# Optimization experiments

Hardware: AMD Instinct MI355X
Metric: run time of the kernel (lower is better)

Reference implementation:

```python
import jax, jax.numpy as jnp
import numpy as np
import math

D_MODEL = 2048
N_HEADS = 16
HEAD_DIM = D_MODEL // N_HEADS
ROPE_THETA = 10000.0
EPS = 1e-5


def _rope_cos_sin(seq_len, dim, theta):
    inv_freq = 1.0 / theta ** (jnp.arange(0, dim, 2, dtype=jnp.float32) / dim)  # [dim/2]
    t = jnp.arange(seq_len, dtype=jnp.float32)
    freqs = jnp.outer(t, inv_freq)  # [S, dim/2]
    return jnp.cos(freqs), jnp.sin(freqs)


def _apply_rope(x, cos, sin):
    # x: [B, S, H, D]; pairs (even, odd) rotated by angle freqs[s, d/2]
    xs = x.reshape(x.shape[:-1] + (x.shape[-1] // 2, 2))
    x0, x1 = xs[..., 0], xs[..., 1]
    c = cos[None, :, None, :]
    s = sin[None, :, None, :]
    out = jnp.stack([x0 * c - x1 * s, x0 * s + x1 * c], axis=-1)
    return out.reshape(x.shape)


def _layernorm(x, w, eps):
    # LayerNorm over last dim, no bias
    mu = jnp.mean(x, axis=-1, keepdims=True)
    var = jnp.mean(jnp.square(x - mu), axis=-1, keepdims=True)
    return (x - mu) * jax.lax.rsqrt(var + eps) * w


def setup_inputs() -> dict:
    key = jax.random.key(0)
    ks = jax.random.split(key, 5)
    B, S = 2, 2048
    w_std = math.sqrt(1.0 / D_MODEL)  # ~xavier for square matrices
    return {
        "x": jax.random.normal(ks[0], (B, S, D_MODEL), dtype=jnp.float32),
        "wq": jax.random.normal(ks[1], (D_MODEL, D_MODEL), dtype=jnp.float32) * w_std,
        "wk": jax.random.normal(ks[2], (D_MODEL, D_MODEL), dtype=jnp.float32) * w_std,
        "wv": jax.random.normal(ks[3], (D_MODEL, D_MODEL), dtype=jnp.float32) * w_std,
        "wo": jax.random.normal(ks[4], (D_MODEL, D_MODEL), dtype=jnp.float32) * w_std,
        "q_norm_w": jnp.ones((HEAD_DIM,), dtype=jnp.float32),
        "k_norm_w": jnp.ones((HEAD_DIM,), dtype=jnp.float32),
        "window_size": 1024,
    }


def reference(x, wq, wk, wv, wo, q_norm_w, k_norm_w, window_size):
    B, S, _ = x.shape
    # bias-free projections (torch Linear: x @ W.T)
    q = (x @ wq.T).reshape(B, S, N_HEADS, HEAD_DIM)
    k = (x @ wk.T).reshape(B, S, N_HEADS, HEAD_DIM)
    v = (x @ wv.T).reshape(B, S, N_HEADS, HEAD_DIM)

    cos, sin = _rope_cos_sin(S, HEAD_DIM, ROPE_THETA)
    q = _apply_rope(q, cos, sin)
    k = _apply_rope(k, cos, sin)

    # per-head QK LayerNorm (no bias)
    q = _layernorm(q, q_norm_w, EPS)
    k = _layernorm(k, k_norm_w, EPS)

    scale = 1.0 / math.sqrt(HEAD_DIM)
    scores = jnp.einsum("bqhd,bkhd->bhqk", q, k) * scale  # [B,H,S,S]

    # sliding-window causal mask: attend to j in [i - window, i]
    i = jnp.arange(S)[:, None]
    j = jnp.arange(S)[None, :]
    allowed = (j <= i) & (j >= i - window_size)
    scores = jnp.where(allowed, scores, -jnp.inf)

    attn = jax.nn.softmax(scores, axis=-1)
    out = jnp.einsum("bhqk,bkhd->bqhd", attn, v).reshape(B, S, D_MODEL)
    return out @ wo.T
```

## Files before the change

kernel.cpp:

```cpp
#include <hip/hip_runtime.h>

typedef __bf16 bfv8 __attribute__((ext_vector_type(8)));
typedef float f32x4 __attribute__((ext_vector_type(4)));

#define DMODEL 2048
#define NHEADS 16
#define HEADD 128
#define SEQ 2048
#define BATCH 2
#define MROWS (BATCH * SEQ)

__device__ __forceinline__ unsigned short f2bf(float f) {
    unsigned int x = __float_as_uint(f);
    x += 0x7fffu + ((x >> 16) & 1u);
    return (unsigned short)(x >> 16);
}
__device__ __forceinline__ float bf2f(unsigned short u) {
    return __uint_as_float((unsigned int)u << 16);
}
__device__ __forceinline__ unsigned int pk2(float a, float b) {
    return (unsigned int)f2bf(a) | ((unsigned int)f2bf(b) << 16);
}

__global__ __launch_bounds__(256) void cvt_all(const float* __restrict__ x,
                                               const float* __restrict__ wq,
                                               const float* __restrict__ wk,
                                               const float* __restrict__ wv,
                                               const float* __restrict__ wo,
                                               unsigned short* __restrict__ dst) {
    int bid = blockIdx.x;
    const float* s;
    int off;
    if (bid < 8192)       { s = x;  off = bid; }
    else if (bid < 12288) { s = wq; off = bid - 8192; }
    else if (bid < 16384) { s = wk; off = bid - 12288; }
    else if (bid < 20480) { s = wv; off = bid - 16384; }
    else                  { s = wo; off = bid - 20480; }
    int i = off * 1024 + threadIdx.x * 4;
    float4 v = *(const float4*)(s + i);
    ushort4 o;
    o.x = f2bf(v.x); o.y = f2bf(v.y); o.z = f2bf(v.z); o.w = f2bf(v.w);
    *(ushort4*)(dst + (size_t)bid * 1024 + threadIdx.x * 4) = o;
}

template <int CPRL, int ITERS>
__device__ __forceinline__ void stage_n(const unsigned short* __restrict__ gbase,
                                        unsigned short* lds, size_t strideShorts,
                                        int wave, int lane) {
#pragma unroll
    for (int i = 0; i < ITERS; ++i) {
        int L = wave * (64 * ITERS) + i * 64 + lane;
        int m = L >> CPRL, c = L & ((1 << CPRL) - 1);
        int g = c ^ (m & 7);
        const unsigned short* gp = gbase + (size_t)m * strideShorts + g * 8;
        __builtin_amdgcn_global_load_lds(
            (const __attribute__((address_space(1))) unsigned int*)gp,
            (__attribute__((address_space(3))) unsigned int*)(lds + (size_t)(wave * (64 * ITERS) + i * 64) * 8),
            16, 0, 0);
    }
}

#define GBK 64

__global__ __launch_bounds__(256) void gemm_qkv(const unsigned short* __restrict__ A,
                                                const unsigned short* __restrict__ Bw,
                                                unsigned short* __restrict__ Qb,
                                                unsigned short* __restrict__ Kb,
                                                unsigned short* __restrict__ VT) {
    __shared__ __align__(16) unsigned short As[128 * 64];
    __shared__ __align__(16) unsigned short Bs[128 * 64];
    const int K = DMODEL;
    int tid  = threadIdx.x;
    int bm   = blockIdx.y * 128, bn = blockIdx.x * 128;
    int wave = tid >> 6, lane = tid & 63;
    int wm   = (wave >> 1) * 64, wn = (wave & 1) * 64;
    int lr   = lane & 15, lg = lane >> 4;

    f32x4 acc[4][4];
    f32x4 z = {0.f, 0.f, 0.f, 0.f};
#pragma unroll
    for (int i = 0; i < 4; ++i)
#pragma unroll
        for (int j = 0; j < 4; ++j) acc[i][j] = z;

    const unsigned short* Ab = A  + (size_t)bm * K;
    const unsigned short* Bb = Bw + (size_t)bn * K;

    for (int k0 = 0; k0 < K; k0 += GBK) {
        __syncthreads();
        stage_n<3, 4>(Ab + k0, As, K, wave, lane);
        stage_n<3, 4>(Bb + k0, Bs, K, wave, lane);
        __syncthreads();
#pragma unroll
        for (int kk = 0; kk < GBK; kk += 32) {
            int ck = (kk >> 3) + lg;
            bfv8 af[4], bf[4];
#pragma unroll
            for (int i = 0; i < 4; ++i)
                af[i] = *(const bfv8*)&As[(wm + i * 16 + lr) * 64 + (ck ^ (lr & 7)) * 8];
#pragma unroll
            for (int j = 0; j < 4; ++j)
                bf[j] = *(const bfv8*)&Bs[(wn + j * 16 + lr) * 64 + (ck ^ (lr & 7)) * 8];
#pragma unroll
            for (int i = 0; i < 4; ++i)
#pragma unroll
                for (int j = 0; j < 4; ++j)
                    acc[i][j] = __builtin_amdgcn_mfma_f32_16x16x32_bf16(af[i], bf[j], acc[i][j], 0, 0, 0);
        }
    }
    int orow0 = bm + wm + lg * 4;
    int region = bn >> 11;
    int nloc   = bn & 2047;
    if (region < 2) {
        unsigned short* C = region ? Kb : Qb;
#pragma unroll
        for (int i = 0; i < 4; ++i)
#pragma unroll
            for (int j = 0; j < 4; ++j)
#pragma unroll
                for (int r = 0; r < 4; ++r)
                    C[(size_t)(orow0 + i * 16 + r) * DMODEL + nloc + wn + j * 16 + lr] = f2bf(acc[i][j][r]);
    } else {
#pragma unroll
        for (int i = 0; i < 4; ++i) {
            int row = orow0 + i * 16;
            int bb = row >> 11, ss = row & (SEQ - 1);
#pragma unroll
            for (int j = 0; j < 4; ++j) {
                int col = nloc + wn + j * 16 + lr;
                int hh = col >> 7, dd = col & (HEADD - 1);
                ushort4 o4;
                o4.x = f2bf(acc[i][j][0]);
                o4.y = f2bf(acc[i][j][1]);
                o4.z = f2bf(acc[i][j][2]);
                o4.w = f2bf(acc[i][j][3]);
                *(ushort4*)(VT + ((size_t)((bb * NHEADS + hh) * HEADD + dd)) * SEQ + ss) = o4;
            }
        }
    }
}

__global__ __launch_bounds__(256) void gemm_bt(const unsigned short* __restrict__ A,
                                               const unsigned short* __restrict__ Bw,
                                               float* __restrict__ C,
                                               int M, int N, int K) {
    __shared__ __align__(16) unsigned short As[128 * 64];
    __shared__ __align__(16) unsigned short Bs[128 * 64];
    int tid  = threadIdx.x;
    int bm   = blockIdx.y * 128, bn = blockIdx.x * 128;
    int wave = tid >> 6, lane = tid & 63;
    int wm   = (wave >> 1) * 64, wn = (wave & 1) * 64;
    int lr   = lane & 15, lg = lane >> 4;

    f32x4 acc[4][4];
    f32x4 z = {0.f, 0.f, 0.f, 0.f};
#pragma unroll
    for (int i = 0; i < 4; ++i)
#pragma unroll
        for (int j = 0; j < 4; ++j) acc[i][j] = z;

    const unsigned short* Ab = A  + (size_t)bm * K;
    const unsigned short* Bb = Bw + (size_t)bn * K;

    for (int k0 = 0; k0 < K; k0 += GBK) {
        __syncthreads();
        stage_n<3, 4>(Ab + k0, As, K, wave, lane);
        stage_n<3, 4>(Bb + k0, Bs, K, wave, lane);
        __syncthreads();
#pragma unroll
        for (int kk = 0; kk < GBK; kk += 32) {
            int ck = (kk >> 3) + lg;
            bfv8 af[4], bf[4];
#pragma unroll
            for (int i = 0; i < 4; ++i)
                af[i] = *(const bfv8*)&As[(wm + i * 16 + lr) * 64 + (ck ^ (lr & 7)) * 8];
#pragma unroll
            for (int j = 0; j < 4; ++j)
                bf[j] = *(const bfv8*)&Bs[(wn + j * 16 + lr) * 64 + (ck ^ (lr & 7)) * 8];
#pragma unroll
            for (int i = 0; i < 4; ++i)
#pragma unroll
                for (int j = 0; j < 4; ++j)
                    acc[i][j] = __builtin_amdgcn_mfma_f32_16x16x32_bf16(af[i], bf[j], acc[i][j], 0, 0, 0);
        }
    }
    int orow0 = bm + wm + lg * 4;
    int ocol0 = bn + wn + lr;
#pragma unroll
    for (int i = 0; i < 4; ++i)
#pragma unroll
        for (int j = 0; j < 4; ++j)
#pragma unroll
            for (int r = 0; r < 4; ++r)
                C[(size_t)(orow0 + i * 16 + r) * N + ocol0 + j * 16] = acc[i][j][r];
}

__global__ __launch_bounds__(256) void rope_ln_ip(unsigned short* __restrict__ qt,
                                                  unsigned short* __restrict__ kt,
                                                  const float* __restrict__ qw,
                                                  const float* __restrict__ kw) {
    int which = blockIdx.y;
    unsigned short* t = which ? kt : qt;
    const float* w = which ? kw : qw;
    float scale = which ? 1.0f : 0.08838834764831845f;
    int gr   = blockIdx.x * 4 + (threadIdx.x >> 6);
    int lane = threadIdx.x & 63;
    int m = gr >> 4;
    int h = gr & 15;
    int s = m & (SEQ - 1);
    unsigned short* p = t + (size_t)m * DMODEL + h * HEADD + lane * 2;
    ushort2 xv = *(const ushort2*)p;
    float x0 = bf2f(xv.x), x1 = bf2f(xv.y);
    float inv = powf(10000.0f, -(float)lane * (1.0f / 64.0f));
    float ang = (float)s * inv;
    float sn, c;
    sincosf(ang, &sn, &c);
    float y0 = x0 * c - x1 * sn;
    float y1 = x0 * sn + x1 * c;
    float sum = y0 + y1;
    float sq  = y0 * y0 + y1 * y1;
#pragma unroll
    for (int o = 32; o >= 1; o >>= 1) {
        sum += __shfl_xor(sum, o);
        sq  += __shfl_xor(sq, o);
    }
    float mu  = sum * (1.0f / 128.0f);
    float var = sq * (1.0f / 128.0f) - mu * mu;
    float rs  = rsqrtf(var + 1e-5f) * scale;
    float2 wv = *(const float2*)(w + lane * 2);
    ushort2 ov;
    ov.x = f2bf((y0 - mu) * rs * wv.x);
    ov.y = f2bf((y1 - mu) * rs * wv.y);
    *(ushort2*)p = ov;
}

#define AQT 64
#define AKT 64

__global__ __launch_bounds__(256) void attn_mfma(const unsigned short* __restrict__ qb,
                                                 const unsigned short* __restrict__ kb,
                                                 const unsigned short* __restrict__ vt,
                                                 unsigned short* __restrict__ ob,
                                                 const int* __restrict__ wptr) {
    __shared__ __align__(16) unsigned short Ks[64 * 128];
    __shared__ __align__(16) unsigned short Vs[128 * 64];
    __shared__ __align__(16) unsigned short Ps[4 * 16 * 64];
    int tid  = threadIdx.x;
    int wq   = tid >> 6, lane = tid & 63;
    int lm   = lane & 15, lg = lane >> 4;
    int lm7  = lm & 7;
    int gid  = blockIdx.x;
    int xcd  = gid & 7, slot = gid >> 3;
    int bh   = xcd * 4 + (slot >> 5);
    int b    = bh >> 4, h = bh & 15;
    int q0   = (31 - (slot & 31)) * AQT;
    int W    = *wptr;
    unsigned short* PsW = &Ps[wq * 1024];

    bfv8 qa[4];
    {
        const unsigned short* qp = qb + (size_t)(b * SEQ + q0 + wq * 16 + lm) * DMODEL + h * HEADD + lg * 8;
#pragma unroll
        for (int kk = 0; kk < 4; ++kk) qa[kk] = *(const bfv8*)(qp + kk * 32);
    }

    f32x4 o[8];
    f32x4 z = {0.f, 0.f, 0.f, 0.f};
#pragma unroll
    for (int n = 0; n < 8; ++n) o[n] = z;
    float mrow = -1e30f, lrow = 0.f;

    const unsigned short* kbase = kb + (size_t)(b * SEQ) * DMODEL + h * HEADD;
    const unsigned short* vbase = vt + (size_t)((b * NHEADS + h) * HEADD) * SEQ;

    int kt_lo = max(0, q0 - W) & ~(AKT - 1);
    int qi = q0 + wq * 16 + lm;

    for (int kt = kt_lo; kt < q0 + AQT; kt += AKT) {
        __syncthreads();
        stage_n<4, 4>(kbase + (size_t)kt * DMODEL, Ks, DMODEL, wq, lane);
        stage_n<3, 4>(vbase + kt, Vs, SEQ, wq, lane);
        __syncthreads();

        f32x4 s[4];
#pragma unroll
        for (int j = 0; j < 4; ++j) s[j] = z;
#pragma unroll
        for (int kk = 0; kk < 4; ++kk) {
#pragma unroll
            for (int j = 0; j < 4; ++j) {
                int ck = (kk * 4 + lg) ^ lm7;
                bfv8 af = *(const bfv8*)&Ks[(j * 16 + lm) * 128 + ck * 8];
                s[j] = __builtin_amdgcn_mfma_f32_16x16x32_bf16(af, qa[kk], s[j], 0, 0, 0);
            }
        }
        if ((kt + 63 >= q0) || (kt < q0 + 63 - W)) {
#pragma unroll
            for (int j = 0; j < 4; ++j) {
                int kj0 = kt + j * 16 + lg * 4;
#pragma unroll
                for (int r = 0; r < 4; ++r) {
                    bool ok = (kj0 + r <= qi) && (kj0 + r >= qi - W);
                    s[j][r] = ok ? s[j][r] : -1e30f;
                }
            }
        }
        float mx = -1e30f;
#pragma unroll
        for (int j = 0; j < 4; ++j)
#pragma unroll
            for (int r = 0; r < 4; ++r) mx = fmaxf(mx, s[j][r]);
        mx = fmaxf(mx, __shfl_xor(mx, 16));
        mx = fmaxf(mx, __shfl_xor(mx, 32));
        float mnew  = fmaxf(mrow, mx);
        float alpha = __expf(mrow - mnew);
        mrow = mnew;
        float ls = 0.f;
#pragma unroll
        for (int j = 0; j < 4; ++j) {
            float p0 = __expf(s[j][0] - mnew);
            float p1 = __expf(s[j][1] - mnew);
            float p2 = __expf(s[j][2] - mnew);
            float p3 = __expf(s[j][3] - mnew);
            ls += (p0 + p1) + (p2 + p3);
            int c0 = (j * 2 + (lg >> 1)) ^ lm7;
            uint2 wv;
            wv.x = pk2(p0, p1);
            wv.y = pk2(p2, p3);
            *(uint2*)&PsW[lm * 64 + c0 * 8 + (lg & 1) * 4] = wv;
        }
        ls += __shfl_xor(ls, 16);
        ls += __shfl_xor(ls, 32);
        lrow = lrow * alpha + ls;
        float al[4];
#pragma unroll
        for (int r = 0; r < 4; ++r) al[r] = __shfl(alpha, lg * 4 + r);
#pragma unroll
        for (int n = 0; n < 8; ++n)
#pragma unroll
            for (int r = 0; r < 4; ++r) o[n][r] *= al[r];
#pragma unroll
        for (int k2 = 0; k2 < 2; ++k2) {
            int cc = (k2 * 4 + lg) ^ lm7;
            bfv8 pa = *(const bfv8*)&PsW[lm * 64 + cc * 8];
#pragma unroll
            for (int n = 0; n < 8; ++n) {
                bfv8 vf = *(const bfv8*)&Vs[(n * 16 + lm) * 64 + cc * 8];
                o[n] = __builtin_amdgcn_mfma_f32_16x16x32_bf16(pa, vf, o[n], 0, 0, 0);
            }
        }
    }
    float linv[4];
#pragma unroll
    for (int r = 0; r < 4; ++r) linv[r] = 1.0f / __shfl(lrow, lg * 4 + r);
    int qrow = q0 + wq * 16 + lg * 4;
    unsigned short* op = ob + (size_t)(b * SEQ + qrow) * DMODEL + h * HEADD + lm;
#pragma unroll
    for (int n = 0; n < 8; ++n)
#pragma unroll
        for (int r = 0; r < 4; ++r)
            op[(size_t)r * DMODEL + n * 16] = f2bf(o[n][r] * linv[r]);
}

extern "C" void kernel_launch(void* const* d_in, const int* in_sizes, int n_in,
                              void* d_out, int out_size, void* d_ws, size_t ws_size,
                              hipStream_t stream) {
    const float* x   = (const float*)d_in[0];
    const float* wq  = (const float*)d_in[1];
    const float* wk  = (const float*)d_in[2];
    const float* wv  = (const float*)d_in[3];
    const float* wo  = (const float*)d_in[4];
    const float* qnw = (const float*)d_in[5];
    const float* knw = (const float*)d_in[6];
    const int*   wsz = (const int*)d_in[7];
    float* out = (float*)d_out;

    char* ws = (char*)d_ws;
    unsigned short* xb  = (unsigned short*)(ws);
    unsigned short* w1  = (unsigned short*)(ws + 16777216);
    unsigned short* w4  = (unsigned short*)(ws + 41943040);
    unsigned short* qbf = (unsigned short*)(ws + 50331648);
    unsigned short* kbf = (unsigned short*)(ws + 67108864);
    unsigned short* vtb = (unsigned short*)(ws + 83886080);

    cvt_all<<<24576, 256, 0, stream>>>(x, wq, wk, wv, wo, xb);

    gemm_qkv<<<dim3(3 * DMODEL / 128, MROWS / 128), 256, 0, stream>>>(xb, w1, qbf, kbf, vtb);

    rope_ln_ip<<<dim3(MROWS * NHEADS / 4, 2), 256, 0, stream>>>(qbf, kbf, qnw, knw);

    attn_mfma<<<(SEQ / AQT) * NHEADS * BATCH, 256, 0, stream>>>(qbf, kbf, vtb, xb, wsz);

    gemm_bt<<<dim3(DMODEL / 128, MROWS / 128), 256, 0, stream>>>(xb, w4, out, MROWS, DMODEL, DMODEL);
}
```

Baseline: 417.2 us.

## Rewrite QKV GEMM with 256x256 tiles and double-buffered async LDS pipeline

The QKV projection GEMM moves from 128x128 tiles with 256 threads and a single LDS buffer to 256x256 tiles with 512 threads. Global-to-LDS loads are double-buffered and interleaved between four MFMA sub-phases, using explicit waitcnt, barriers, sched_barrier and setprio to overlap memory traffic with matrix math. The aim is to hide load latency and raise arithmetic intensity per tile. In exchange it uses much more LDS and registers per block, and the grid shrinks to 384 blocks, which can leave a partial second wave across the CUs.

```diff
diff --git a/kernel.cpp b/kernel.cpp
--- a/kernel.cpp
+++ b/kernel.cpp
@@ -61,60 +61,143 @@
 }
 
 #define GBK 64
-
-__global__ __launch_bounds__(256) void gemm_qkv(const unsigned short* __restrict__ A,
-                                                const unsigned short* __restrict__ Bw,
-                                                unsigned short* __restrict__ Qb,
-                                                unsigned short* __restrict__ Kb,
-                                                unsigned short* __restrict__ VT) {
-    __shared__ __align__(16) unsigned short As[128 * 64];
-    __shared__ __align__(16) unsigned short Bs[128 * 64];
+#define QNT (DMODEL / 64)
+
+__global__ __launch_bounds__(512, 2) void gemm_qkv(const unsigned short* __restrict__ A,
+                                                   const unsigned short* __restrict__ Bw,
+                                                   unsigned short* __restrict__ Qb,
+                                                   unsigned short* __restrict__ Kb,
+                                                   unsigned short* __restrict__ VT) {
+    __shared__ __align__(16) unsigned short LA[2][256 * 64];
+    __shared__ __align__(16) unsigned short LB[2][256 * 64];
     const int K = DMODEL;
     int tid  = threadIdx.x;
-    int bm   = blockIdx.y * 128, bn = blockIdx.x * 128;
     int wave = tid >> 6, lane = tid & 63;
-    int wm   = (wave >> 1) * 64, wn = (wave & 1) * 64;
-    int lr   = lane & 15, lg = lane >> 4;
-
-    f32x4 acc[4][4];
-    f32x4 z = {0.f, 0.f, 0.f, 0.f};
-#pragma unroll
-    for (int i = 0; i < 4; ++i)
-#pragma unroll
-        for (int j = 0; j < 4; ++j) acc[i][j] = z;
+    int wr = wave >> 2, wc = wave & 3;
+    int wm = wr * 128, wn = wc * 64;
+    int lr = lane & 15, lg = lane >> 4, lsw = lr & 7;
+    int bm = blockIdx.y * 256, bn = blockIdx.x * 256;
 
     const unsigned short* Ab = A  + (size_t)bm * K;
     const unsigned short* Bb = Bw + (size_t)bn * K;
 
-    for (int k0 = 0; k0 < K; k0 += GBK) {
-        __syncthreads();
-        stage_n<3, 4>(Ab + k0, As, K, wave, lane);
-        stage_n<3, 4>(Bb + k0, Bs, K, wave, lane);
-        __syncthreads();
-#pragma unroll
-        for (int kk = 0; kk < GBK; kk += 32) {
-            int ck = (kk >> 3) + lg;
-            bfv8 af[4], bf[4];
-#pragma unroll
-            for (int i = 0; i < 4; ++i)
-                af[i] = *(const bfv8*)&As[(wm + i * 16 + lr) * 64 + (ck ^ (lr & 7)) * 8];
-#pragma unroll
-            for (int j = 0; j < 4; ++j)
-                bf[j] = *(const bfv8*)&Bs[(wn + j * 16 + lr) * 64 + (ck ^ (lr & 7)) * 8];
-#pragma unroll
-            for (int i = 0; i < 4; ++i)
-#pragma unroll
-                for (int j = 0; j < 4; ++j)
-                    acc[i][j] = __builtin_amdgcn_mfma_f32_16x16x32_bf16(af[i], bf[j], acc[i][j], 0, 0, 0);
-        }
-    }
+    f32x4 acc[8][4];
+    f32x4 z = {0.f, 0.f, 0.f, 0.f};
+#pragma unroll
+    for (int i = 0; i < 8; ++i)
+#pragma unroll
+        for (int j = 0; j < 4; ++j) acc[i][j] = z;
+
+    stage_n<3, 2>(Ab,                        LA[0],            K, wave, lane);
+    stage_n<3, 2>(Ab + (size_t)128 * K,      LA[0] + 128 * 64, K, wave, lane);
+    stage_n<3, 2>(Bb,                        LB[0],            K, wave, lane);
+    stage_n<3, 2>(Bb + (size_t)128 * K,      LB[0] + 128 * 64, K, wave, lane);
+    stage_n<3, 2>(Ab + 64,                   LA[1],            K, wave, lane);
+    stage_n<3, 2>(Ab + (size_t)128 * K + 64, LA[1] + 128 * 64, K, wave, lane);
+    asm volatile("s_waitcnt vmcnt(4)" ::: "memory");
+    __builtin_amdgcn_s_barrier();
+    __builtin_amdgcn_sched_barrier(0);
+
+#pragma unroll 2
+    for (int t = 0; t < QNT; ++t) {
+        const unsigned short* As = LA[t & 1];
+        const unsigned short* Bs = LB[t & 1];
+        unsigned short* AsN = LA[t & 1];
+        unsigned short* BsN = LB[(t & 1) ^ 1];
+        int tA = t + 2; if (tA >= QNT) tA = t;
+        int tB = t + 1; if (tB >= QNT) tB = t - 1;
+
+        bfv8 a03[4][2], a47[4][2], b01[2][2], b23[2][2];
+
+        stage_n<3, 2>(Bb + (size_t)tB * 64, BsN, K, wave, lane);
+#pragma unroll
+        for (int i = 0; i < 4; ++i)
+#pragma unroll
+            for (int ks = 0; ks < 2; ++ks)
+                a03[i][ks] = *(const bfv8*)&As[(wm + i * 16 + lr) * 64 + ((ks * 4 + lg) ^ lsw) * 8];
+#pragma unroll
+        for (int j = 0; j < 2; ++j)
+#pragma unroll
+            for (int ks = 0; ks < 2; ++ks)
+                b01[j][ks] = *(const bfv8*)&Bs[(wn + j * 16 + lr) * 64 + ((ks * 4 + lg) ^ lsw) * 8];
+        __builtin_amdgcn_sched_barrier(0);
+        __builtin_amdgcn_s_setprio(1);
+#pragma unroll
+        for (int i = 0; i < 4; ++i)
+#pragma unroll
+            for (int j = 0; j < 2; ++j)
+#pragma unroll
+                for (int ks = 0; ks < 2; ++ks)
+                    acc[i][j] = __builtin_amdgcn_mfma_f32_16x16x32_bf16(a03[i][ks], b01[j][ks], acc[i][j], 0, 0, 0);
+        __builtin_amdgcn_s_setprio(0);
+        __builtin_amdgcn_sched_barrier(0);
+
+        stage_n<3, 2>(Bb + (size_t)128 * K + tB * 64, BsN + 128 * 64, K, wave, lane);
+#pragma unroll
+        for (int i = 0; i < 4; ++i)
+#pragma unroll
+            for (int ks = 0; ks < 2; ++ks)
+                a47[i][ks] = *(const bfv8*)&As[(wm + 64 + i * 16 + lr) * 64 + ((ks * 4 + lg) ^ lsw) * 8];
+#pragma unroll
+        for (int j = 0; j < 2; ++j)
+#pragma unroll
+            for (int ks = 0; ks < 2; ++ks)
+                b23[j][ks] = *(const bfv8*)&Bs[(wn + 32 + j * 16 + lr) * 64 + ((ks * 4 + lg) ^ lsw) * 8];
+        __builtin_amdgcn_sched_barrier(0);
+        __builtin_amdgcn_s_setprio(1);
+#pragma unroll
+        for (int i = 0; i < 4; ++i)
+#pragma unroll
+            for (int j = 0; j < 2; ++j)
+#pragma unroll
+                for (int ks = 0; ks < 2; ++ks)
+                    acc[i][2 + j] = __builtin_amdgcn_mfma_f32_16x16x32_bf16(a03[i][ks], b23[j][ks], acc[i][2 + j], 0, 0, 0);
+        __builtin_amdgcn_s_setprio(0);
+        __builtin_amdgcn_sched_barrier(0);
+
+        asm volatile("s_waitcnt lgkmcnt(0)" ::: "memory");
+        __builtin_amdgcn_s_barrier();
+        __builtin_amdgcn_sched_barrier(0);
+
+        stage_n<3, 2>(Ab + (size_t)tA * 64, AsN, K, wave, lane);
+        __builtin_amdgcn_sched_barrier(0);
+        __builtin_amdgcn_s_setprio(1);
+#pragma unroll
+        for (int i = 0; i < 4; ++i)
+#pragma unroll
+            for (int j = 0; j < 2; ++j)
+#pragma unroll
+                for (int ks = 0; ks < 2; ++ks)
+                    acc[4 + i][j] = __builtin_amdgcn_mfma_f32_16x16x32_bf16(a47[i][ks], b01[j][ks], acc[4 + i][j], 0, 0, 0);
+        __builtin_amdgcn_s_setprio(0);
+        __builtin_amdgcn_sched_barrier(0);
+
+        stage_n<3, 2>(Ab + (size_t)128 * K + tA * 64, AsN + 128 * 64, K, wave, lane);
+        __builtin_amdgcn_sched_barrier(0);
+        __builtin_amdgcn_s_setprio(1);
+#pragma unroll
+        for (int i = 0; i < 4; ++i)
+#pragma unroll
+            for (int j = 0; j < 2; ++j)
+#pragma unroll
+                for (int ks = 0; ks < 2; ++ks)
+                    acc[4 + i][2 + j] = __builtin_amdgcn_mfma_f32_16x16x32_bf16(a47[i][ks], b23[j][ks], acc[4 + i][2 + j], 0, 0, 0);
+        __builtin_amdgcn_s_setprio(0);
+        __builtin_amdgcn_sched_barrier(0);
+
+        asm volatile("s_waitcnt vmcnt(4)" ::: "memory");
+        __builtin_amdgcn_s_barrier();
+        __builtin_amdgcn_sched_barrier(0);
+    }
+    asm volatile("s_waitcnt vmcnt(0)" ::: "memory");
+
     int orow0 = bm + wm + lg * 4;
     int region = bn >> 11;
     int nloc   = bn & 2047;
     if (region < 2) {
         unsigned short* C = region ? Kb : Qb;
 #pragma unroll
-        for (int i = 0; i < 4; ++i)
+        for (int i = 0; i < 8; ++i)
 #pragma unroll
             for (int j = 0; j < 4; ++j)
 #pragma unroll
@@ -122,7 +205,7 @@
                     C[(size_t)(orow0 + i * 16 + r) * DMODEL + nloc + wn + j * 16 + lr] = f2bf(acc[i][j][r]);
     } else {
 #pragma unroll
-        for (int i = 0; i < 4; ++i) {
+        for (int i = 0; i < 8; ++i) {
             int row = orow0 + i * 16;
             int bb = row >> 11, ss = row & (SEQ - 1);
 #pragma unroll
@@ -385,7 +468,7 @@
 
     cvt_all<<<24576, 256, 0, stream>>>(x, wq, wk, wv, wo, xb);
 
-    gemm_qkv<<<dim3(3 * DMODEL / 128, MROWS / 128), 256, 0, stream>>>(xb, w1, qbf, kbf, vtb);
+    gemm_qkv<<<dim3(3 * DMODEL / 256, MROWS / 256), 512, 0, stream>>>(xb, w1, qbf, kbf, vtb);
 
     rope_ln_ip<<<dim3(MROWS * NHEADS / 4, 2), 256, 0, stream>>>(qbf, kbf, qnw, knw);
 
```

Result: no change. 423.6 us (+1.5%).

## Rewrite QKV GEMM as 256x256 tile with multi-stage async LDS pipeline

Applied to the files above, without the earlier changes.

The QKV projection GEMM moves from 128x128 tiles with 4 waves and a load/sync/compute loop to 256x256 tiles with 8 waves. It uses a double-buffered, k-split LDS ring with direct global-to-LDS loads issued one phase ahead. Barriers use explicit vmcnt/lgkmcnt waits and setprio around the MFMA bursts so that memory traffic overlaps compute. The larger tile raises data reuse per load, but it needs 128 KB of LDS and 128 accumulator registers per thread, and the grid shrinks to 384 blocks, which may hurt occupancy and tail balance.

```diff
diff --git a/kernel.cpp b/kernel.cpp
--- a/kernel.cpp
+++ b/kernel.cpp
@@ -60,61 +60,119 @@
     }
 }
 
+template <int ITERS>
+__device__ __forceinline__ void stage_k(const unsigned short* __restrict__ gbase,
+                                        unsigned short* lds, int strideShorts,
+                                        int wave, int lane) {
+#pragma unroll
+    for (int i = 0; i < ITERS; ++i) {
+        int L = wave * (64 * ITERS) + i * 64 + lane;
+        int m = L >> 2, c = L & 3;
+        int g = c ^ ((m >> 2) & 3);
+        const unsigned short* gp = gbase + (size_t)m * strideShorts + g * 8;
+        __builtin_amdgcn_global_load_lds(
+            (const __attribute__((address_space(1))) unsigned int*)gp,
+            (__attribute__((address_space(3))) unsigned int*)(lds + (size_t)(wave * (64 * ITERS) + i * 64) * 8),
+            16, 0, 0);
+    }
+}
+
 #define GBK 64
-
-__global__ __launch_bounds__(256) void gemm_qkv(const unsigned short* __restrict__ A,
-                                                const unsigned short* __restrict__ Bw,
-                                                unsigned short* __restrict__ Qb,
-                                                unsigned short* __restrict__ Kb,
-                                                unsigned short* __restrict__ VT) {
-    __shared__ __align__(16) unsigned short As[128 * 64];
-    __shared__ __align__(16) unsigned short Bs[128 * 64];
+#define QNT (DMODEL / 64)
+
+#define PHASE(SLOT, KS, IH, READB, STDST, STSRC)                                        \
+    do {                                                                                \
+        stage_k<2>((STSRC), (STDST), K, wave, lane);                                    \
+        if (READB) {                                                                    \
+            _Pragma("unroll") for (int j = 0; j < 4; ++j)                               \
+                bf[j] = *(const bfv8*)&L[SLOT][2 + KS][(wn + j * 16 + lr) * 32 + coff]; \
+        }                                                                               \
+        _Pragma("unroll") for (int i = 0; i < 4; ++i)                                   \
+            af[i] = *(const bfv8*)&L[SLOT][KS][(wm + (IH) * 64 + i * 16 + lr) * 32 + coff]; \
+        __builtin_amdgcn_sched_barrier(0);                                              \
+        __builtin_amdgcn_s_barrier();                                                   \
+        asm volatile("s_waitcnt lgkmcnt(0)" ::: "memory");                              \
+        __builtin_amdgcn_sched_barrier(0);                                              \
+        __builtin_amdgcn_s_setprio(1);                                                  \
+        _Pragma("unroll") for (int i = 0; i < 4; ++i)                                   \
+            _Pragma("unroll") for (int j = 0; j < 4; ++j)                               \
+                acc[(IH) * 4 + i][j] = __builtin_amdgcn_mfma_f32_16x16x32_bf16(         \
+                    af[i], bf[j], acc[(IH) * 4 + i][j], 0, 0, 0);                       \
+        __builtin_amdgcn_s_setprio(0);                                                  \
+        __builtin_amdgcn_sched_barrier(0);                                              \
+    } while (0)
+
+#define BAR_ODD                           \
+    __builtin_amdgcn_s_barrier();         \
+    __builtin_amdgcn_sched_barrier(0);
+
+#define BAR_EVEN                                        \
+    asm volatile("s_waitcnt vmcnt(8)" ::: "memory");    \
+    __builtin_amdgcn_s_barrier();                       \
+    __builtin_amdgcn_sched_barrier(0);
+
+__global__ __launch_bounds__(512, 2) void gemm_qkv(const unsigned short* __restrict__ A,
+                                                   const unsigned short* __restrict__ Bw,
+                                                   unsigned short* __restrict__ Qb,
+                                                   unsigned short* __restrict__ Kb,
+                                                   unsigned short* __restrict__ VT) {
+    __shared__ __align__(16) unsigned short L[2][4][256 * 32];
     const int K = DMODEL;
     int tid  = threadIdx.x;
-    int bm   = blockIdx.y * 128, bn = blockIdx.x * 128;
     int wave = tid >> 6, lane = tid & 63;
-    int wm   = (wave >> 1) * 64, wn = (wave & 1) * 64;
-    int lr   = lane & 15, lg = lane >> 4;
-
-    f32x4 acc[4][4];
-    f32x4 z = {0.f, 0.f, 0.f, 0.f};
-#pragma unroll
-    for (int i = 0; i < 4; ++i)
-#pragma unroll
-        for (int j = 0; j < 4; ++j) acc[i][j] = z;
+    int wr = wave >> 2, wc = wave & 3;
+    int wm = wr * 128, wn = wc * 64;
+    int lr = lane & 15, lg = lane >> 4;
+    int coff = (lg ^ ((lr >> 2) & 3)) * 8;
+    int bm = blockIdx.y * 256, bn = blockIdx.x * 256;
 
     const unsigned short* Ab = A  + (size_t)bm * K;
     const unsigned short* Bb = Bw + (size_t)bn * K;
 
-    for (int k0 = 0; k0 < K; k0 += GBK) {
-        __syncthreads();
-        stage_n<3, 4>(Ab + k0, As, K, wave, lane);
-        stage_n<3, 4>(Bb + k0, Bs, K, wave, lane);
-        __syncthreads();
-#pragma unroll
-        for (int kk = 0; kk < GBK; kk += 32) {
-            int ck = (kk >> 3) + lg;
-            bfv8 af[4], bf[4];
-#pragma unroll
-            for (int i = 0; i < 4; ++i)
-                af[i] = *(const bfv8*)&As[(wm + i * 16 + lr) * 64 + (ck ^ (lr & 7)) * 8];
-#pragma unroll
-            for (int j = 0; j < 4; ++j)
-                bf[j] = *(const bfv8*)&Bs[(wn + j * 16 + lr) * 64 + (ck ^ (lr & 7)) * 8];
-#pragma unroll
-            for (int i = 0; i < 4; ++i)
-#pragma unroll
-                for (int j = 0; j < 4; ++j)
-                    acc[i][j] = __builtin_amdgcn_mfma_f32_16x16x32_bf16(af[i], bf[j], acc[i][j], 0, 0, 0);
-        }
-    }
+    f32x4 acc[8][4];
+    f32x4 z = {0.f, 0.f, 0.f, 0.f};
+#pragma unroll
+    for (int i = 0; i < 8; ++i)
+#pragma unroll
+        for (int j = 0; j < 4; ++j) acc[i][j] = z;
+
+    stage_k<2>(Ab,      &L[0][0][0], K, wave, lane);
+    stage_k<2>(Bb,      &L[0][2][0], K, wave, lane);
+    stage_k<2>(Ab + 32, &L[0][1][0], K, wave, lane);
+    stage_k<2>(Bb + 32, &L[0][3][0], K, wave, lane);
+    stage_k<2>(Ab + 64, &L[1][0][0], K, wave, lane);
+    stage_k<2>(Bb + 64, &L[1][2][0], K, wave, lane);
+    asm volatile("s_waitcnt vmcnt(8)" ::: "memory");
+    __builtin_amdgcn_s_barrier();
+    __builtin_amdgcn_sched_barrier(0);
+
+    bfv8 af[4], bf[4];
+
+#pragma unroll 1
+    for (int it = 0; it < QNT / 2; ++it) {
+        int u  = 2 * it;
+        int t1 = u + 1;
+        int t2 = (u + 2 < QNT) ? u + 2 : QNT - 1;
+        int t3 = (u + 3 < QNT) ? u + 3 : QNT - 1;
+
+        PHASE(0, 0, 0, true,  &L[1][1][0], Ab + (size_t)t1 * 64 + 32); BAR_ODD;
+        PHASE(0, 0, 1, false, &L[1][3][0], Bb + (size_t)t1 * 64 + 32); BAR_EVEN;
+        PHASE(0, 1, 0, true,  &L[0][0][0], Ab + (size_t)t2 * 64);      BAR_ODD;
+        PHASE(0, 1, 1, false, &L[0][2][0], Bb + (size_t)t2 * 64);      BAR_EVEN;
+        PHASE(1, 0, 0, true,  &L[0][1][0], Ab + (size_t)t2 * 64 + 32); BAR_ODD;
+        PHASE(1, 0, 1, false, &L[0][3][0], Bb + (size_t)t2 * 64 + 32); BAR_EVEN;
+        PHASE(1, 1, 0, true,  &L[1][0][0], Ab + (size_t)t3 * 64);      BAR_ODD;
+        PHASE(1, 1, 1, false, &L[1][2][0], Bb + (size_t)t3 * 64);      BAR_EVEN;
+    }
+    asm volatile("s_waitcnt vmcnt(0)" ::: "memory");
+
     int orow0 = bm + wm + lg * 4;
     int region = bn >> 11;
     int nloc   = bn & 2047;
     if (region < 2) {
         unsigned short* C = region ? Kb : Qb;
 #pragma unroll
-        for (int i = 0; i < 4; ++i)
+        for (int i = 0; i < 8; ++i)
 #pragma unroll
             for (int j = 0; j < 4; ++j)
 #pragma unroll
@@ -122,7 +180,7 @@
                     C[(size_t)(orow0 + i * 16 + r) * DMODEL + nloc + wn + j * 16 + lr] = f2bf(acc[i][j][r]);
     } else {
 #pragma unroll
-        for (int i = 0; i < 4; ++i) {
+        for (int i = 0; i < 8; ++i) {
             int row = orow0 + i * 16;
             int bb = row >> 11, ss = row & (SEQ - 1);
 #pragma unroll
@@ -385,7 +443,7 @@
 
     cvt_all<<<24576, 256, 0, stream>>>(x, wq, wk, wv, wo, xb);
 
-    gemm_qkv<<<dim3(3 * DMODEL / 128, MROWS / 128), 256, 0, stream>>>(xb, w1, qbf, kbf, vtb);
+    gemm_qkv<<<dim3(3 * DMODEL / 256, MROWS / 256), 512, 0, stream>>>(xb, w1, qbf, kbf, vtb);
 
     rope_ln_ip<<<dim3(MROWS * NHEADS / 4, 2), 256, 0, stream>>>(qbf, kbf, qnw, knw);
 
```

Result: no change. 421.8 us (+1.1%).

## Enlarge QKV GEMM tiles and double-buffer LDS with async prefetch

Applied to the files above, without the earlier changes.

Rewrites the fused QKV projection GEMM to use 512-thread blocks computing 256x192 output tiles with 8x3 MFMA accumulators per wave. A and B are double-buffered in LDS, and the next K-slices are prefetched with global_load_lds under explicit waitcnt and barriers. MFMA phases are raised with s_setprio. The aim is to hide global load latency and raise data reuse per LDS load. In exchange it uses much more LDS and registers, which can limit occupancy, and the 192-wide tiles require the Q/K/V region selection to move into the per-column epilogue.

```diff
diff --git a/kernel.cpp b/kernel.cpp
--- a/kernel.cpp
+++ b/kernel.cpp
@@ -61,74 +61,112 @@
 }
 
 #define GBK 64
-
-__global__ __launch_bounds__(256) void gemm_qkv(const unsigned short* __restrict__ A,
-                                                const unsigned short* __restrict__ Bw,
-                                                unsigned short* __restrict__ Qb,
-                                                unsigned short* __restrict__ Kb,
-                                                unsigned short* __restrict__ VT) {
-    __shared__ __align__(16) unsigned short As[128 * 64];
-    __shared__ __align__(16) unsigned short Bs[128 * 64];
+#define QNT (DMODEL / 64)
+
+__global__ __launch_bounds__(512, 2) void gemm_qkv(const unsigned short* __restrict__ A,
+                                                   const unsigned short* __restrict__ Bw,
+                                                   unsigned short* __restrict__ Qb,
+                                                   unsigned short* __restrict__ Kb,
+                                                   unsigned short* __restrict__ VT) {
+    __shared__ __align__(16) unsigned short LA[2][256 * 64];
+    __shared__ __align__(16) unsigned short LB[2][192 * 64];
     const int K = DMODEL;
     int tid  = threadIdx.x;
-    int bm   = blockIdx.y * 128, bn = blockIdx.x * 128;
     int wave = tid >> 6, lane = tid & 63;
-    int wm   = (wave >> 1) * 64, wn = (wave & 1) * 64;
-    int lr   = lane & 15, lg = lane >> 4;
-
-    f32x4 acc[4][4];
-    f32x4 z = {0.f, 0.f, 0.f, 0.f};
-#pragma unroll
-    for (int i = 0; i < 4; ++i)
-#pragma unroll
-        for (int j = 0; j < 4; ++j) acc[i][j] = z;
+    int wr = wave >> 2, wc = wave & 3;
+    int wm = wr * 128, wn = wc * 48;
+    int lr = lane & 15, lg = lane >> 4, lsw = lr & 7;
+    int bm = blockIdx.y * 256, bn = blockIdx.x * 192;
 
     const unsigned short* Ab = A  + (size_t)bm * K;
     const unsigned short* Bb = Bw + (size_t)bn * K;
 
-    for (int k0 = 0; k0 < K; k0 += GBK) {
-        __syncthreads();
-        stage_n<3, 4>(Ab + k0, As, K, wave, lane);
-        stage_n<3, 4>(Bb + k0, Bs, K, wave, lane);
-        __syncthreads();
-#pragma unroll
-        for (int kk = 0; kk < GBK; kk += 32) {
-            int ck = (kk >> 3) + lg;
-            bfv8 af[4], bf[4];
-#pragma unroll
-            for (int i = 0; i < 4; ++i)
-                af[i] = *(const bfv8*)&As[(wm + i * 16 + lr) * 64 + (ck ^ (lr & 7)) * 8];
-#pragma unroll
-            for (int j = 0; j < 4; ++j)
-                bf[j] = *(const bfv8*)&Bs[(wn + j * 16 + lr) * 64 + (ck ^ (lr & 7)) * 8];
-#pragma unroll
-            for (int i = 0; i < 4; ++i)
-#pragma unroll
-                for (int j = 0; j < 4; ++j)
-                    acc[i][j] = __builtin_amdgcn_mfma_f32_16x16x32_bf16(af[i], bf[j], acc[i][j], 0, 0, 0);
-        }
-    }
+    f32x4 acc[8][3];
+    f32x4 z = {0.f, 0.f, 0.f, 0.f};
+#pragma unroll
+    for (int i = 0; i < 8; ++i)
+#pragma unroll
+        for (int j = 0; j < 3; ++j) acc[i][j] = z;
+
+    stage_n<3, 4>(Ab,      LA[0], K, wave, lane);
+    stage_n<3, 3>(Bb,      LB[0], K, wave, lane);
+    stage_n<3, 4>(Ab + 64, LA[1], K, wave, lane);
+    asm volatile("s_waitcnt vmcnt(4)" ::: "memory");
+    __builtin_amdgcn_s_barrier();
+    __builtin_amdgcn_sched_barrier(0);
+
+    bfv8 a[8], b[3];
+
+#pragma unroll 2
+    for (int t = 0; t < QNT; ++t) {
+        const unsigned short* As = LA[t & 1];
+        const unsigned short* Bs = LB[t & 1];
+        unsigned short* AsN = LA[t & 1];
+        unsigned short* BsN = LB[(t & 1) ^ 1];
+        int tB = (t + 1 < QNT) ? t + 1 : QNT - 1;
+        int tA = (t + 2 < QNT) ? t + 2 : QNT - 1;
+
+        stage_n<3, 3>(Bb + (size_t)tB * 64, BsN, K, wave, lane);
+#pragma unroll
+        for (int i = 0; i < 8; ++i)
+            a[i] = *(const bfv8*)&As[(wm + i * 16 + lr) * 64 + (lg ^ lsw) * 8];
+#pragma unroll
+        for (int j = 0; j < 3; ++j)
+            b[j] = *(const bfv8*)&Bs[(wn + j * 16 + lr) * 64 + (lg ^ lsw) * 8];
+        __builtin_amdgcn_sched_barrier(0);
+        __builtin_amdgcn_s_setprio(1);
+#pragma unroll
+        for (int i = 0; i < 8; ++i)
+#pragma unroll
+            for (int j = 0; j < 3; ++j)
+                acc[i][j] = __builtin_amdgcn_mfma_f32_16x16x32_bf16(a[i], b[j], acc[i][j], 0, 0, 0);
+        __builtin_amdgcn_s_setprio(0);
+        __builtin_amdgcn_sched_barrier(0);
+
+#pragma unroll
+        for (int i = 0; i < 8; ++i)
+            a[i] = *(const bfv8*)&As[(wm + i * 16 + lr) * 64 + ((4 + lg) ^ lsw) * 8];
+#pragma unroll
+        for (int j = 0; j < 3; ++j)
+            b[j] = *(const bfv8*)&Bs[(wn + j * 16 + lr) * 64 + ((4 + lg) ^ lsw) * 8];
+        __builtin_amdgcn_sched_barrier(0);
+        __builtin_amdgcn_s_setprio(1);
+#pragma unroll
+        for (int i = 0; i < 8; ++i)
+#pragma unroll
+            for (int j = 0; j < 3; ++j)
+                acc[i][j] = __builtin_amdgcn_mfma_f32_16x16x32_bf16(a[i], b[j], acc[i][j], 0, 0, 0);
+        __builtin_amdgcn_s_setprio(0);
+        __builtin_amdgcn_sched_barrier(0);
+
+        asm volatile("s_waitcnt lgkmcnt(0)" ::: "memory");
+        __builtin_amdgcn_s_barrier();
+        __builtin_amdgcn_sched_barrier(0);
+
+        stage_n<3, 4>(Ab + (size_t)tA * 64, AsN, K, wave, lane);
+        asm volatile("s_waitcnt vmcnt(4)" ::: "memory");
+        __builtin_amdgcn_s_barrier();
+        __builtin_amdgcn_sched_barrier(0);
+    }
+    asm volatile("s_waitcnt vmcnt(0)" ::: "memory");
+
     int orow0 = bm + wm + lg * 4;
-    int region = bn >> 11;
-    int nloc   = bn & 2047;
-    if (region < 2) {
-        unsigned short* C = region ? Kb : Qb;
-#pragma unroll
-        for (int i = 0; i < 4; ++i)
-#pragma unroll
-            for (int j = 0; j < 4; ++j)
+#pragma unroll
+    for (int i = 0; i < 8; ++i) {
+        int row = orow0 + i * 16;
+        int bb = row >> 11, ss = row & (SEQ - 1);
+#pragma unroll
+        for (int j = 0; j < 3; ++j) {
+            int col0 = bn + wn + j * 16;
+            int region = col0 >> 11;
+            if (region < 2) {
+                unsigned short* C = region ? Kb : Qb;
 #pragma unroll
                 for (int r = 0; r < 4; ++r)
-                    C[(size_t)(orow0 + i * 16 + r) * DMODEL + nloc + wn + j * 16 + lr] = f2bf(acc[i][j][r]);
-    } else {
-#pragma unroll
-        for (int i = 0; i < 4; ++i) {
-            int row = orow0 + i * 16;
-            int bb = row >> 11, ss = row & (SEQ - 1);
-#pragma unroll
-            for (int j = 0; j < 4; ++j) {
-                int col = nloc + wn + j * 16 + lr;
-                int hh = col >> 7, dd = col & (HEADD - 1);
+                    C[(size_t)(row + r) * DMODEL + (col0 & 2047) + lr] = f2bf(acc[i][j][r]);
+            } else {
+                int colf = col0 + lr;
+                int hh = (colf >> 7) & 15, dd = colf & (HEADD - 1);
                 ushort4 o4;
                 o4.x = f2bf(acc[i][j][0]);
                 o4.y = f2bf(acc[i][j][1]);
@@ -385,7 +423,7 @@
 
     cvt_all<<<24576, 256, 0, stream>>>(x, wq, wk, wv, wo, xb);
 
-    gemm_qkv<<<dim3(3 * DMODEL / 128, MROWS / 128), 256, 0, stream>>>(xb, w1, qbf, kbf, vtb);
+    gemm_qkv<<<dim3(3 * DMODEL / 192, MROWS / 256), 512, 0, stream>>>(xb, w1, qbf, kbf, vtb);
 
     rope_ln_ip<<<dim3(MROWS * NHEADS / 4, 2), 256, 0, stream>>>(qbf, kbf, qnw, knw);
 
```

Result: no change. 411.7 us (-1.3%).
